# Optimization experiments

Measured on AMD Instinct MI355X. Metric: run time of the kernel, lower is better.

Reference implementation:

```python
import jax, jax.numpy as jnp
import numpy as np

N = 50000      # nodes
E = 800000     # edges (before self-loops)
DIN, H1, H2, OUT = 128, 128, 64, 40
LN_EPS = 1e-5


def setup_inputs() -> dict:
    key = jax.random.key(0)
    ks = jax.random.split(key, 16)
    s = lambda d: 1.0 / np.sqrt(d)
    inp = {
        "x": jax.random.normal(ks[0], (N, DIN), jnp.float32),
        "edge_index": jax.random.randint(ks[1], (2, E), 0, N, dtype=jnp.int64),
        # GCNConv weights (applied as x @ W) and biases
        "W1": jax.random.normal(ks[2], (DIN, H1), jnp.float32) * s(DIN),
        "b1": jnp.zeros((H1,), jnp.float32),
        "W2": jax.random.normal(ks[3], (H1, H2), jnp.float32) * s(H1),
        "b2": jnp.zeros((H2,), jnp.float32),
        "W3": jax.random.normal(ks[4], (H2, H2), jnp.float32) * s(H2),
        "b3": jnp.zeros((H2,), jnp.float32),
        # LayerNorms
        "g1": jnp.ones((H1,), jnp.float32),
        "be1": jnp.zeros((H1,), jnp.float32),
        "g2": jnp.ones((H2,), jnp.float32),
        "be2": jnp.zeros((H2,), jnp.float32),
        # post_mp MLP head
        "Wp1": jax.random.normal(ks[5], (H2, H2), jnp.float32) * s(H2),
        "bp1": jnp.zeros((H2,), jnp.float32),
        "Wp2": jax.random.normal(ks[6], (H2, OUT), jnp.float32) * s(H2),
        "bp2": jnp.zeros((OUT,), jnp.float32),
    }
    return inp


def _layer_norm(x, g, b):
    mu = jnp.mean(x, axis=-1, keepdims=True)
    var = jnp.mean((x - mu) ** 2, axis=-1, keepdims=True)
    return (x - mu) * jax.lax.rsqrt(var + LN_EPS) * g + b


def _gcn(x, src, dst, norm, W, b):
    # PyG GCNConv: linear first, then normalized gather/scatter-add, bias last
    h = x @ W                                  # [N, H]
    msg = h[src] * norm[:, None]               # [E+N, H] gather
    out = jax.ops.segment_sum(msg, dst, num_segments=N)  # scatter-add
    return out + b


def reference(x, edge_index, W1, b1, W2, b2, W3, b3, g1, be1, g2, be2,
              Wp1, bp1, Wp2, bp2):
    loops = jnp.arange(N, dtype=edge_index.dtype)
    src = jnp.concatenate([edge_index[0], loops])  # add self-loops
    dst = jnp.concatenate([edge_index[1], loops])
    # symmetric normalization D^{-1/2} (A+I) D^{-1/2} (same graph all layers)
    deg = jax.ops.segment_sum(jnp.ones_like(src, dtype=x.dtype), dst,
                              num_segments=N)
    dinv = jnp.where(deg > 0, jax.lax.rsqrt(jnp.maximum(deg, 1.0)), 0.0)
    norm = dinv[src] * dinv[dst]

    h = _gcn(x, src, dst, norm, W1, b1)
    h = _layer_norm(jax.nn.relu(h), g1, be1)
    h = _gcn(h, src, dst, norm, W2, b2)
    h = _layer_norm(jax.nn.relu(h), g2, be2)
    emb = _gcn(h, src, dst, norm, W3, b3)      # emb = conv output, pre-ReLU
    h = jax.nn.relu(emb)
    h = (h @ Wp1 + bp1) @ Wp2 + bp2            # post_mp: two stacked Linears
    return emb, jax.nn.log_softmax(h, axis=1)
```

## Files before the change

### kernel.cpp

```cpp
#include <hip/hip_runtime.h>
#include <hip/hip_bf16.h>

#define DIN 128
#define HID1 128
#define HID2 64
#define OUTD 40
#define NCHUNK 128

typedef __attribute__((ext_vector_type(8))) short bf16x8;
typedef __attribute__((ext_vector_type(4))) float f32x4;

__device__ __forceinline__ float bf2f(unsigned int u) {
    union { unsigned int i; float f; } c;
    c.i = u << 16;
    return c.f;
}
__device__ __forceinline__ unsigned short f2bf(float f) {
    union { float f; unsigned int i; } c; c.f = f;
    unsigned int r = c.i + 0x7FFFu + ((c.i >> 16) & 1u);
    return (unsigned short)(r >> 16);
}
__device__ __forceinline__ unsigned int packbf(float lo, float hi) {
    return (unsigned int)f2bf(lo) | ((unsigned int)f2bf(hi) << 16);
}

__device__ __forceinline__ int get_src(const int* ei, int E, int e, int e64) {
    return e64 ? ei[2 * e] : ei[e];
}
__device__ __forceinline__ int get_dst(const int* ei, int E, int e, int e64) {
    return e64 ? ei[2 * (E + e)] : ei[E + e];
}

struct WCvt {
    const void* p[14];
    int sz[14];
    int off[14];
    int tobf[14];
    int cols[14];
};

__launch_bounds__(1024)
__global__ void posA_kernel(const unsigned short* __restrict__ xu,
                            const int* __restrict__ ei,
                            int* __restrict__ flags,
                            int* __restrict__ pos,
                            unsigned int* __restrict__ hist,
                            int E, int N) {
    __shared__ unsigned int h32[25000];
    __shared__ int sh2[2];
    const int NW = (N + 1) >> 1;
    const int b = blockIdx.x;
    const int t = threadIdx.x;
    if (b < NCHUNK) {
        if (t == 0) sh2[0] = 0;
        for (int w = t; w < NW; w += 1024) h32[w] = 0u;
        __syncthreads();
        int zodd = 0;
        for (int k = t; k < 1024; k += 1024)
            if (ei[2 * k + 1] == 0) zodd++;
        if (zodd) atomicAdd(&sh2[0], zodd);
        __syncthreads();
        const int e64 = (sh2[0] > 512) ? 1 : 0;
        const int CH = (E + NCHUNK - 1) / NCHUNK;
        const int lo = b * CH;
        int hi = lo + CH; if (hi > E) hi = E;
        for (int e = lo + t; e < hi; e += 1024) {
            int d = e64 ? ei[2 * (E + e)] : ei[E + e];
            if ((unsigned)d < (unsigned)N) {
                unsigned sh = (unsigned)(d & 1) << 4;
                unsigned old = atomicAdd(&h32[d >> 1], 1u << sh);
                pos[e] = (int)((old >> sh) & 0xffffu);
            } else {
                pos[e] = -1;
            }
        }
        __syncthreads();
        unsigned int* hb = hist + (size_t)b * NW;
        for (int w = t; w < NW; w += 1024) hb[w] = h32[w];
    } else {
        if (t < 2) sh2[t] = 0;
        __syncthreads();
        int bad = 0;
        for (int k = t; k < 2048; k += 1024) {
            float v = bf2f(xu[2 * k]);
            float a = fabsf(v);
            if (!(a <= 1e4f) || (v != 0.f && a < 1e-4f)) bad++;
        }
        int zodd = 0;
        for (int k = t; k < 1024; k += 1024)
            if (ei[2 * k + 1] == 0) zodd++;
        if (bad) atomicAdd(&sh2[0], bad);
        if (zodd) atomicAdd(&sh2[1], zodd);
        __syncthreads();
        if (t == 0) {
            flags[0] = (sh2[0] > 512) ? 1 : 0;
            flags[1] = (sh2[1] > 512) ? 1 : 0;
        }
    }
}

__launch_bounds__(256)
__global__ void phaseB_kernel(const unsigned int* __restrict__ hist,
                              unsigned int* __restrict__ basev,
                              int* __restrict__ cnt, int* __restrict__ bsum,
                              int N, int PB,
                              WCvt wc, unsigned short* __restrict__ wbf,
                              float* __restrict__ wf,
                              const int* __restrict__ flags) {
    __shared__ int red[256];
    const int NW = (N + 1) >> 1;
    int t = threadIdx.x;
    int blk = blockIdx.x;
    if (blk < PB) {
        int w = blk * 256 + t;
        unsigned run0 = 0, run1 = 0;
        if (w < NW) {
            #pragma unroll 4
            for (int b = 0; b < NCHUNK; ++b) {
                unsigned u = hist[(size_t)b * NW + w];
                basev[(size_t)b * NW + w] = (run0 & 0xffffu) | (run1 << 16);
                run0 += u & 0xffffu;
                run1 += u >> 16;
            }
            cnt[2 * w] = (int)run0;
            if (2 * w + 1 < N) cnt[2 * w + 1] = (int)run1;
        }
        int tot = 0;
        if (w < NW) tot = (int)run0 + ((2 * w + 1 < N) ? (int)run1 : 0);
        red[t] = tot;
        __syncthreads();
        #pragma unroll
        for (int off = 64; off >= 1; off >>= 1) {
            if ((t & 127) < off) red[t] += red[t + off];
            __syncthreads();
        }
        if (t == 0) bsum[2 * blk] = red[0];
        if (t == 128) bsum[2 * blk + 1] = red[128];
    } else {
        int xf32 = flags[0];
        int stride = (gridDim.x - PB) * 256;
        int tid = (blk - PB) * 256 + t;
        for (int a = 0; a < 14; ++a) {
            const float* pf = (const float*)wc.p[a];
            const unsigned short* pb = (const unsigned short*)wc.p[a];
            int n = wc.sz[a], off = wc.off[a], tobf = wc.tobf[a];
            int cols = wc.cols[a];
            int rows = tobf ? (n / cols) : 0;
            for (int i = tid; i < n; i += stride) {
                float v = xf32 ? pf[i] : bf2f(pb[i]);
                if (tobf) {
                    int k = i / cols, m = i % cols;
                    wbf[off + m * rows + k] = f2bf(v);
                } else {
                    wf[off + i] = v;
                }
            }
        }
    }
}

__launch_bounds__(256)
__global__ void emit_kernel(const int* __restrict__ cnt, const int* __restrict__ bsum,
                            int* __restrict__ indptr, float* __restrict__ dinv,
                            int N, int NB) {
    __shared__ int part[256];
    __shared__ int sh[256];
    int t = threadIdx.x;
    part[t] = (t < NB) ? bsum[t] : 0;
    __syncthreads();
    for (int off = 1; off < 256; off <<= 1) {
        int v = (t >= off) ? part[t - off] : 0;
        __syncthreads();
        part[t] += v;
        __syncthreads();
    }
    int bbase = (blockIdx.x > 0) ? part[blockIdx.x - 1] : 0;
    int total = part[255];
    int i = blockIdx.x * 256 + t;
    int c = (i < N) ? cnt[i] : 0;
    sh[t] = c;
    __syncthreads();
    for (int off = 1; off < 256; off <<= 1) {
        int v = (t >= off) ? sh[t - off] : 0;
        __syncthreads();
        sh[t] += v;
        __syncthreads();
    }
    if (i < N) {
        int excl = sh[t] - c + bbase;
        indptr[i] = excl;
        dinv[i] = 1.0f / sqrtf((float)(c + 1));
    }
    if (blockIdx.x == (unsigned)(NB - 1) && t == 0) indptr[N] = total;
}

__global__ void scatter_kernel(const int* __restrict__ ei, const int* __restrict__ indptr,
                               const int* __restrict__ pos, const float* __restrict__ dinv,
                               const unsigned int* __restrict__ basev,
                               int2* __restrict__ csr_sn,
                               int E, int N, const int* __restrict__ flags) {
    int e64 = flags[1];
    int CH = (E + NCHUNK - 1) / NCHUNK;
    int NW = (N + 1) >> 1;
    int base = (blockIdx.x * blockDim.x + threadIdx.x) * 4;
    #pragma unroll
    for (int u = 0; u < 4; ++u) {
        int e = base + u;
        if (e < E) {
            int p = pos[e];
            if (p >= 0) {
                int bb = e / CH;
                int d = get_dst(ei, E, e, e64);
                int s = get_src(ei, E, e, e64);
                if ((unsigned)s >= (unsigned)N) s = 0;
                float nrm = dinv[s] * dinv[d];
                unsigned bw = basev[(size_t)bb * NW + (d >> 1)];
                int bval = (d & 1) ? (int)(bw >> 16) : (int)(bw & 0xffffu);
                int slot = indptr[d] + bval + p;
                csr_sn[slot] = make_int2(s, __float_as_int(nrm));
            }
        }
    }
}


template<typename AT>
__device__ __forceinline__ bf16x8 ld_afrag(const AT* p);
template<>
__device__ __forceinline__ bf16x8 ld_afrag<unsigned short>(const unsigned short* p) {
    return *(const bf16x8*)p;
}
template<>
__device__ __forceinline__ bf16x8 ld_afrag<float>(const float* p) {
    float4 a = *(const float4*)p;
    float4 b = *(const float4*)(p + 4);
    bf16x8 r;
    r[0] = (short)f2bf(a.x); r[1] = (short)f2bf(a.y);
    r[2] = (short)f2bf(a.z); r[3] = (short)f2bf(a.w);
    r[4] = (short)f2bf(b.x); r[5] = (short)f2bf(b.y);
    r[6] = (short)f2bf(b.z); r[7] = (short)f2bf(b.w);
    return r;
}

template<int K, int M, typename AT>
__device__ __forceinline__ void mm_body(const AT* __restrict__ A,
                                        const unsigned short* __restrict__ WT,
                                        unsigned short* __restrict__ C, int N,
                                        unsigned short (*Ws)[K + 8]) {
    int tid = threadIdx.x;
    for (int idx = tid; idx < M * K / 8; idx += 256) {
        int r = idx / (K / 8), c8 = idx % (K / 8);
        *(uint4*)&Ws[r][c8 * 8] = *(const uint4*)&WT[r * K + c8 * 8];
    }
    __syncthreads();
    int w = tid >> 6, lane = tid & 63;
    int m = lane & 15, q = lane >> 4;
    int row_a = blockIdx.x * 64 + w * 16 + m;
    if (row_a >= N) row_a = N - 1;
    const AT* arow = A + (size_t)row_a * K;
    f32x4 acc[M / 16];
    #pragma unroll
    for (int t = 0; t < M / 16; ++t) acc[t] = (f32x4){0.f, 0.f, 0.f, 0.f};
    #pragma unroll
    for (int ks = 0; ks < K / 32; ++ks) {
        int k0 = ks * 32 + q * 8;
        bf16x8 a = ld_afrag<AT>(arow + k0);
        #pragma unroll
        for (int t = 0; t < M / 16; ++t) {
            bf16x8 b = *(const bf16x8*)&Ws[t * 16 + m][k0];
            acc[t] = __builtin_amdgcn_mfma_f32_16x16x32_bf16(a, b, acc[t], 0, 0, 0);
        }
    }
    int rbase = blockIdx.x * 64 + w * 16 + q * 4;
    #pragma unroll
    for (int reg = 0; reg < 4; ++reg) {
        int row = rbase + reg;
        if (row < N) {
            #pragma unroll
            for (int t = 0; t < M / 16; ++t)
                C[(size_t)row * M + t * 16 + m] = f2bf(acc[t][reg]);
        }
    }
}

template<int K, int M>
__launch_bounds__(256)
__global__ void mm_dual_kernel(const void* __restrict__ A,
                               const unsigned short* __restrict__ WT,
                               unsigned short* __restrict__ C, int N,
                               const int* __restrict__ flags) {
    __shared__ unsigned short Ws[M][K + 8];
    if (flags[0]) mm_body<K, M, float>((const float*)A, WT, C, N, Ws);
    else          mm_body<K, M, unsigned short>((const unsigned short*)A, WT, C, N, Ws);
}

template<int K, int M>
__launch_bounds__(256)
__global__ void mm_bf_kernel(const unsigned short* __restrict__ A,
                             const unsigned short* __restrict__ WT,
                             unsigned short* __restrict__ C, int N) {
    __shared__ unsigned short Ws[M][K + 8];
    mm_body<K, M, unsigned short>(A, WT, C, N, Ws);
}


template<int VPL>
__device__ __forceinline__ void gacc1(float* acc, const unsigned short* r, float n) {
    if constexpr (VPL == 8) {
        uint4 u = *(const uint4*)r;
        acc[0] += bf2f(u.x & 0xffffu) * n; acc[1] += bf2f(u.x >> 16) * n;
        acc[2] += bf2f(u.y & 0xffffu) * n; acc[3] += bf2f(u.y >> 16) * n;
        acc[4] += bf2f(u.z & 0xffffu) * n; acc[5] += bf2f(u.z >> 16) * n;
        acc[6] += bf2f(u.w & 0xffffu) * n; acc[7] += bf2f(u.w >> 16) * n;
    } else {
        uint2 u = *(const uint2*)r;
        acc[0] += bf2f(u.x & 0xffffu) * n; acc[1] += bf2f(u.x >> 16) * n;
        acc[2] += bf2f(u.y & 0xffffu) * n; acc[3] += bf2f(u.y >> 16) * n;
    }
}

template<int VPL>
__device__ __forceinline__ void gacc8(float* acc,
                                      const unsigned short* const* rp,
                                      const float* nv) {
    if constexpr (VPL == 8) {
        uint4 u[8];
        #pragma unroll
        for (int i = 0; i < 8; ++i) u[i] = *(const uint4*)rp[i];
        #pragma unroll
        for (int i = 0; i < 8; ++i) {
            float n = nv[i];
            acc[0] += bf2f(u[i].x & 0xffffu) * n; acc[1] += bf2f(u[i].x >> 16) * n;
            acc[2] += bf2f(u[i].y & 0xffffu) * n; acc[3] += bf2f(u[i].y >> 16) * n;
            acc[4] += bf2f(u[i].z & 0xffffu) * n; acc[5] += bf2f(u[i].z >> 16) * n;
            acc[6] += bf2f(u[i].w & 0xffffu) * n; acc[7] += bf2f(u[i].w >> 16) * n;
        }
    } else {
        uint2 u[8];
        #pragma unroll
        for (int i = 0; i < 8; ++i) u[i] = *(const uint2*)rp[i];
        #pragma unroll
        for (int i = 0; i < 8; ++i) {
            float n = nv[i];
            acc[0] += bf2f(u[i].x & 0xffffu) * n; acc[1] += bf2f(u[i].x >> 16) * n;
            acc[2] += bf2f(u[i].y & 0xffffu) * n; acc[3] += bf2f(u[i].y >> 16) * n;
        }
    }
}

template<int H, bool RELU_LN, bool EMB>
__launch_bounds__(256)
__global__ void agg_kernel(const unsigned short* __restrict__ h,
                           const int* __restrict__ indptr,
                           const int2* __restrict__ csr_sn,
                           const float* __restrict__ dinv,
                           const float* __restrict__ bias,
                           const float* __restrict__ gamma,
                           const float* __restrict__ beta,
                           unsigned short* __restrict__ out,
                           void* __restrict__ out_emb,
                           int N, const int* __restrict__ flags) {
    constexpr int VPL = H / 16;
    __shared__ int2 lsn[4][4][32];
    int w = threadIdx.x >> 6;
    int lane = threadIdx.x & 63;
    int g = lane >> 4;
    int idx = lane & 15;
    int node = blockIdx.x * 16 + w * 4 + g;
    bool active = node < N;
    int nd = active ? node : N - 1;
    float di = dinv[nd];
    int c0 = idx * VPL;
    float acc[VPL];
    #pragma unroll
    for (int v = 0; v < VPL; ++v) acc[v] = 0.f;
    gacc1<VPL>(acc, h + (size_t)nd * H + c0, di * di);
    int beg = indptr[nd], end = indptr[nd + 1];
    for (int base = beg; base < end; base += 32) {
        int m = end - base; if (m > 32) m = 32;
        lsn[w][g][idx]      = (idx < m)      ? csr_sn[base + idx]      : make_int2(0, 0);
        lsn[w][g][idx + 16] = (idx + 16 < m) ? csr_sn[base + idx + 16] : make_int2(0, 0);
        int rounds = (m + 7) >> 3;
        int j = 0;
        for (int rr = 0; rr < rounds; ++rr, j += 8) {
            const unsigned short* rp[8];
            float nv[8];
            #pragma unroll
            for (int i = 0; i < 8; ++i) {
                int2 e = lsn[w][g][j + i];
                rp[i] = h + (size_t)e.x * H + c0;
                nv[i] = __int_as_float(e.y);
            }
            gacc8<VPL>(acc, rp, nv);
        }
    }
    #pragma unroll
    for (int v = 0; v < VPL; ++v) acc[v] += bias[c0 + v];
    if constexpr (RELU_LN) {
        #pragma unroll
        for (int v = 0; v < VPL; ++v) acc[v] = fmaxf(acc[v], 0.f);
        float s = 0.f, sq = 0.f;
        #pragma unroll
        for (int v = 0; v < VPL; ++v) { s += acc[v]; sq += acc[v] * acc[v]; }
        #pragma unroll
        for (int off = 8; off >= 1; off >>= 1) {
            s += __shfl_xor(s, off, 64);
            sq += __shfl_xor(sq, off, 64);
        }
        float mu = s * (1.0f / H);
        float var = fmaxf(sq * (1.0f / H) - mu * mu, 0.f);
        float inv = 1.0f / sqrtf(var + 1e-5f);
        #pragma unroll
        for (int v = 0; v < VPL; ++v)
            acc[v] = (acc[v] - mu) * inv * gamma[c0 + v] + beta[c0 + v];
    }
    if (active) {
        unsigned short* orow = out + (size_t)node * H + c0;
        if constexpr (VPL == 8) {
            uint4 p;
            p.x = packbf(acc[0], acc[1]); p.y = packbf(acc[2], acc[3]);
            p.z = packbf(acc[4], acc[5]); p.w = packbf(acc[6], acc[7]);
            *(uint4*)orow = p;
        } else {
            uint2 p; p.x = packbf(acc[0], acc[1]); p.y = packbf(acc[2], acc[3]);
            *(uint2*)orow = p;
        }
        if constexpr (EMB) {
            if (flags[0]) {
                float* o = (float*)out_emb + (size_t)node * H + c0;
                #pragma unroll
                for (int v4 = 0; v4 < VPL / 4; ++v4)
                    *(float4*)(o + v4 * 4) = make_float4(acc[v4 * 4], acc[v4 * 4 + 1],
                                                         acc[v4 * 4 + 2], acc[v4 * 4 + 3]);
            } else {
                unsigned short* o = (unsigned short*)out_emb + (size_t)node * H + c0;
                #pragma unroll
                for (int v2 = 0; v2 < VPL / 2; ++v2)
                    ((unsigned int*)o)[v2] = packbf(acc[v2 * 2], acc[v2 * 2 + 1]);
            }
        }
    }
}


__launch_bounds__(256)
__global__ void head_kernel(const unsigned short* __restrict__ emb,
                            const float* __restrict__ Wp1,
                            const float* __restrict__ bp1,
                            const float* __restrict__ Wp2,
                            const float* __restrict__ bp2,
                            void* __restrict__ d_out, int N,
                            const int* __restrict__ flags) {
    __shared__ float Est[64][68];
    __shared__ float W1s[64][64];
    __shared__ float Tst[64][68];
    __shared__ float W2s[64][OUTD];
    __shared__ float b1s[64];
    __shared__ float b2s[OUTD];
    int tid = threadIdx.x;
    int row0 = blockIdx.x * 64;
    for (int i = tid; i < 64 * 64; i += 256) W1s[i >> 6][i & 63] = Wp1[i];
    for (int i = tid; i < 64 * OUTD; i += 256) W2s[i / OUTD][i % OUTD] = Wp2[i];
    if (tid < 64) b1s[tid] = bp1[tid];
    if (tid < OUTD) b2s[tid] = bp2[tid];
    for (int i = tid; i < 64 * 32; i += 256) {
        int r = i >> 5, kk = i & 31;
        int row = row0 + r;
        unsigned int u = (row < N) ? *(const unsigned int*)&emb[(size_t)row * 64 + kk * 2] : 0u;
        Est[kk * 2][r]     = fmaxf(bf2f(u & 0xffffu), 0.f);
        Est[kk * 2 + 1][r] = fmaxf(bf2f(u >> 16), 0.f);
    }
    __syncthreads();
    {
        int rg = tid >> 4, cg = tid & 15;
        int r = rg * 4, c = cg * 4;
        float acc[4][4];
        #pragma unroll
        for (int i = 0; i < 4; ++i)
            #pragma unroll
            for (int jj = 0; jj < 4; ++jj) acc[i][jj] = b1s[c + jj];
        #pragma unroll 4
        for (int k = 0; k < 64; ++k) {
            float4 a = *(const float4*)&Est[k][r];
            float4 wv = *(const float4*)&W1s[k][c];
            acc[0][0] += a.x * wv.x; acc[0][1] += a.x * wv.y; acc[0][2] += a.x * wv.z; acc[0][3] += a.x * wv.w;
            acc[1][0] += a.y * wv.x; acc[1][1] += a.y * wv.y; acc[1][2] += a.y * wv.z; acc[1][3] += a.y * wv.w;
            acc[2][0] += a.z * wv.x; acc[2][1] += a.z * wv.y; acc[2][2] += a.z * wv.z; acc[2][3] += a.z * wv.w;
            acc[3][0] += a.w * wv.x; acc[3][1] += a.w * wv.y; acc[3][2] += a.w * wv.z; acc[3][3] += a.w * wv.w;
        }
        #pragma unroll
        for (int i = 0; i < 4; ++i)
            #pragma unroll
            for (int jj = 0; jj < 4; ++jj) Tst[c + jj][r + i] = acc[i][jj];
    }
    __syncthreads();
    int row = tid >> 2, tc = tid & 3, o0 = tc * 10;
    int node = row0 + row;
    float u[10];
    #pragma unroll
    for (int o = 0; o < 10; ++o) u[o] = b2s[o0 + o];
    for (int c2 = 0; c2 < 64; ++c2) {
        float tv = Tst[c2][row];
        const float2* wp = (const float2*)&W2s[c2][o0];
        #pragma unroll
        for (int o2 = 0; o2 < 5; ++o2) {
            float2 wv = wp[o2];
            u[o2 * 2]     += tv * wv.x;
            u[o2 * 2 + 1] += tv * wv.y;
        }
    }
    float mx = u[0];
    #pragma unroll
    for (int o = 1; o < 10; ++o) mx = fmaxf(mx, u[o]);
    mx = fmaxf(mx, __shfl_xor(mx, 1, 64));
    mx = fmaxf(mx, __shfl_xor(mx, 2, 64));
    float sum = 0.f;
    #pragma unroll
    for (int o = 0; o < 10; ++o) sum += __expf(u[o] - mx);
    sum += __shfl_xor(sum, 1, 64);
    sum += __shfl_xor(sum, 2, 64);
    float lse = mx + __logf(sum);
    if (node < N) {
        if (flags[0]) {
            float* base = (float*)d_out + (size_t)N * HID2;
            float* op = base + (size_t)node * OUTD + o0;
            #pragma unroll
            for (int o = 0; o < 10; ++o) op[o] = u[o] - lse;
        } else {
            unsigned short* base = (unsigned short*)d_out + (size_t)N * HID2;
            unsigned int* op = (unsigned int*)(base + (size_t)node * OUTD + o0);
            #pragma unroll
            for (int o2 = 0; o2 < 5; ++o2)
                op[o2] = packbf(u[o2 * 2] - lse, u[o2 * 2 + 1] - lse);
        }
    }
}


extern "C" void kernel_launch(void* const* d_in, const int* in_sizes, int n_in,
                              void* d_out, int out_size, void* d_ws, size_t ws_size,
                              hipStream_t stream) {
    const unsigned short* xu = (const unsigned short*)d_in[0];
    const int*            ei = (const int*)d_in[1];

    const int N = in_sizes[0] / DIN;
    const int E = in_sizes[1] / 2;
    const int NW = (N + 1) / 2;

    size_t off = 0;
    auto take = [&](size_t bytes) {
        size_t cur = off;
        off += (bytes + 255) & ~(size_t)255;
        return cur;
    };
    char* ws = (char*)d_ws;
    int*   flags   = (int*)  (ws + take(256));
    int*   cnt     = (int*)  (ws + take((size_t)N * 4));
    float* dinv    = (float*)(ws + take((size_t)N * 4));
    int*   indptr  = (int*)  (ws + take((size_t)(N + 1) * 4));
    int*   pos     = (int*)  (ws + take((size_t)E * 4));
    int2*  csr_sn  = (int2*) (ws + take((size_t)E * 8));
    int*   bsum    = (int*)  (ws + take(((size_t)N / 256 + 4) * 4));
    unsigned int* hist  = (unsigned int*)(ws + take((size_t)NCHUNK * NW * 4));
    unsigned int* basev = (unsigned int*)(ws + take((size_t)NCHUNK * NW * 4));
    unsigned short* wbf = (unsigned short*)(ws + take(32768 * 2));
    float*          wf  = (float*)         (ws + take(8192 * 4));
    unsigned short* hbuf = (unsigned short*)(ws + take((size_t)N * DIN * 2));
    unsigned short* abuf = (unsigned short*)(ws + take((size_t)N * DIN * 2));
    (void)ws_size; (void)n_in; (void)out_size;

    const int TB = 256;
    dim3 blk(TB);
    const int NB = (N + 255) / 256;
    const int PB = (NW + 255) / 256;

    WCvt wc;
    int bfoff = 0, foff = 0;
    int offs[14];
    const int wcols[14] = {HID1, 0, HID2, 0, HID2, 0, 0, 0, 0, 0, 0, 0, 0, 0};
    for (int a = 0; a < 14; ++a) {
        int idx = a + 2;
        wc.p[a] = d_in[idx];
        wc.sz[a] = in_sizes[idx];
        int tobf = (idx == 2 || idx == 4 || idx == 6) ? 1 : 0;
        wc.tobf[a] = tobf;
        wc.cols[a] = tobf ? wcols[a] : 1;
        if (tobf) { wc.off[a] = bfoff; bfoff += in_sizes[idx]; }
        else      { wc.off[a] = foff;  foff  += in_sizes[idx]; }
        offs[a] = wc.off[a];
    }

    posA_kernel<<<dim3(NCHUNK + 1), dim3(1024), 0, stream>>>(
        xu, ei, flags, pos, hist, E, N);
    phaseB_kernel<<<dim3(PB + 64), blk, 0, stream>>>(
        hist, basev, cnt, bsum, N, PB, wc, wbf, wf, flags);
    emit_kernel<<<dim3(NB), blk, 0, stream>>>(cnt, bsum, indptr, dinv, N, NB);
    scatter_kernel<<<dim3((E + 1023) / 1024), blk, 0, stream>>>(
        ei, indptr, pos, dinv, basev, csr_sn, E, N, flags);

    unsigned short* W1t = wbf + offs[0];
    unsigned short* W2t = wbf + offs[2];
    unsigned short* W3t = wbf + offs[4];
    float* b1f  = wf + offs[1];
    float* b2f  = wf + offs[3];
    float* b3f  = wf + offs[5];
    float* g1f  = wf + offs[6];
    float* be1f = wf + offs[7];
    float* g2f  = wf + offs[8];
    float* be2f = wf + offs[9];
    float* Wp1f = wf + offs[10];
    float* bp1f = wf + offs[11];
    float* Wp2f = wf + offs[12];
    float* bp2f = wf + offs[13];

    const int MMG = (N + 63) / 64;
    const int AGG = (N + 15) / 16;

    mm_dual_kernel<DIN, HID1><<<dim3(MMG), blk, 0, stream>>>(
        d_in[0], W1t, hbuf, N, flags);
    agg_kernel<HID1, true, false><<<dim3(AGG), blk, 0, stream>>>(
        hbuf, indptr, csr_sn, dinv, b1f, g1f, be1f, abuf, nullptr, N, flags);

    mm_bf_kernel<HID1, HID2><<<dim3(MMG), blk, 0, stream>>>(abuf, W2t, hbuf, N);
    agg_kernel<HID2, true, false><<<dim3(AGG), blk, 0, stream>>>(
        hbuf, indptr, csr_sn, dinv, b2f, g2f, be2f, abuf, nullptr, N, flags);

    mm_bf_kernel<HID2, HID2><<<dim3(MMG), blk, 0, stream>>>(abuf, W3t, hbuf, N);
    agg_kernel<HID2, false, true><<<dim3(AGG), blk, 0, stream>>>(
        hbuf, indptr, csr_sn, dinv, b3f, nullptr, nullptr, abuf, d_out, N, flags);

    head_kernel<<<dim3((N + 63) / 64), blk, 0, stream>>>(
        abuf, Wp1f, bp1f, Wp2f, bp2f, d_out, N, flags);
}
```

Measured before the change: 278.4 us.

## Assign one wavefront per node in GCN aggregation with edge-split lanes

The aggregation kernel now gives each node a full 64-lane wavefront instead of a 16-lane group. The four 16-lane slots each process a strided subset of the neighbour list with software-pipelined row loads, and the partials are combined by cross-slot shuffles. This is meant to balance work across nodes with uneven degree and to keep more gathers in flight per node. The cost is four times as many blocks, an extra shuffle reduction, and three quarters of the lanes sitting idle during the epilogue and writes.

Measured after the change: 310.6 us. +11.6%, slower.

```diff
diff --git a/kernel.cpp b/kernel.cpp
--- a/kernel.cpp
+++ b/kernel.cpp
@@ -305,46 +305,22 @@
 
 
 template<int VPL>
-__device__ __forceinline__ void gacc1(float* acc, const unsigned short* r, float n) {
+__device__ __forceinline__ uint4 ld_row(const unsigned short* p) {
     if constexpr (VPL == 8) {
-        uint4 u = *(const uint4*)r;
-        acc[0] += bf2f(u.x & 0xffffu) * n; acc[1] += bf2f(u.x >> 16) * n;
-        acc[2] += bf2f(u.y & 0xffffu) * n; acc[3] += bf2f(u.y >> 16) * n;
+        return *(const uint4*)p;
+    } else {
+        uint2 t = *(const uint2*)p;
+        return make_uint4(t.x, t.y, 0u, 0u);
+    }
+}
+
+template<int VPL>
+__device__ __forceinline__ void acc_row(float* acc, uint4 u, float n) {
+    acc[0] += bf2f(u.x & 0xffffu) * n; acc[1] += bf2f(u.x >> 16) * n;
+    acc[2] += bf2f(u.y & 0xffffu) * n; acc[3] += bf2f(u.y >> 16) * n;
+    if constexpr (VPL == 8) {
         acc[4] += bf2f(u.z & 0xffffu) * n; acc[5] += bf2f(u.z >> 16) * n;
         acc[6] += bf2f(u.w & 0xffffu) * n; acc[7] += bf2f(u.w >> 16) * n;
-    } else {
-        uint2 u = *(const uint2*)r;
-        acc[0] += bf2f(u.x & 0xffffu) * n; acc[1] += bf2f(u.x >> 16) * n;
-        acc[2] += bf2f(u.y & 0xffffu) * n; acc[3] += bf2f(u.y >> 16) * n;
-    }
-}
-
-template<int VPL>
-__device__ __forceinline__ void gacc8(float* acc,
-                                      const unsigned short* const* rp,
-                                      const float* nv) {
-    if constexpr (VPL == 8) {
-        uint4 u[8];
-        #pragma unroll
-        for (int i = 0; i < 8; ++i) u[i] = *(const uint4*)rp[i];
-        #pragma unroll
-        for (int i = 0; i < 8; ++i) {
-            float n = nv[i];
-            acc[0] += bf2f(u[i].x & 0xffffu) * n; acc[1] += bf2f(u[i].x >> 16) * n;
-            acc[2] += bf2f(u[i].y & 0xffffu) * n; acc[3] += bf2f(u[i].y >> 16) * n;
-            acc[4] += bf2f(u[i].z & 0xffffu) * n; acc[5] += bf2f(u[i].z >> 16) * n;
-            acc[6] += bf2f(u[i].w & 0xffffu) * n; acc[7] += bf2f(u[i].w >> 16) * n;
-        }
-    } else {
-        uint2 u[8];
-        #pragma unroll
-        for (int i = 0; i < 8; ++i) u[i] = *(const uint2*)rp[i];
-        #pragma unroll
-        for (int i = 0; i < 8; ++i) {
-            float n = nv[i];
-            acc[0] += bf2f(u[i].x & 0xffffu) * n; acc[1] += bf2f(u[i].x >> 16) * n;
-            acc[2] += bf2f(u[i].y & 0xffffu) * n; acc[3] += bf2f(u[i].y >> 16) * n;
-        }
     }
 }
 
@@ -361,12 +337,12 @@
                            void* __restrict__ out_emb,
                            int N, const int* __restrict__ flags) {
     constexpr int VPL = H / 16;
-    __shared__ int2 lsn[4][4][32];
+    __shared__ int2 lsn[4][64];
     int w = threadIdx.x >> 6;
     int lane = threadIdx.x & 63;
-    int g = lane >> 4;
+    int slot = lane >> 4;
     int idx = lane & 15;
-    int node = blockIdx.x * 16 + w * 4 + g;
+    int node = blockIdx.x * 4 + w;
     bool active = node < N;
     int nd = active ? node : N - 1;
     float di = dinv[nd];
@@ -374,25 +350,29 @@
     float acc[VPL];
     #pragma unroll
     for (int v = 0; v < VPL; ++v) acc[v] = 0.f;
-    gacc1<VPL>(acc, h + (size_t)nd * H + c0, di * di);
+    if (slot == 0)
+        acc_row<VPL>(acc, ld_row<VPL>(h + (size_t)nd * H + c0), di * di);
     int beg = indptr[nd], end = indptr[nd + 1];
-    for (int base = beg; base < end; base += 32) {
-        int m = end - base; if (m > 32) m = 32;
-        lsn[w][g][idx]      = (idx < m)      ? csr_sn[base + idx]      : make_int2(0, 0);
-        lsn[w][g][idx + 16] = (idx + 16 < m) ? csr_sn[base + idx + 16] : make_int2(0, 0);
-        int rounds = (m + 7) >> 3;
-        int j = 0;
-        for (int rr = 0; rr < rounds; ++rr, j += 8) {
-            const unsigned short* rp[8];
-            float nv[8];
-            #pragma unroll
-            for (int i = 0; i < 8; ++i) {
-                int2 e = lsn[w][g][j + i];
-                rp[i] = h + (size_t)e.x * H + c0;
-                nv[i] = __int_as_float(e.y);
-            }
-            gacc8<VPL>(acc, rp, nv);
-        }
+    for (int base = beg; base < end; base += 64) {
+        int m = end - base; if (m > 64) m = 64;
+        lsn[w][lane] = (lane < m) ? csr_sn[base + lane] : make_int2(0, 0);
+        int rounds = (m + 3) >> 2;
+        int2 e = lsn[w][slot];
+        uint4 u = ld_row<VPL>(h + (size_t)e.x * H + c0);
+        float n = __int_as_float(e.y);
+        for (int r = 1; r < rounds; ++r) {
+            int2 e2 = lsn[w][r * 4 + slot];
+            uint4 u2 = ld_row<VPL>(h + (size_t)e2.x * H + c0);
+            float n2 = __int_as_float(e2.y);
+            acc_row<VPL>(acc, u, n);
+            u = u2; n = n2;
+        }
+        acc_row<VPL>(acc, u, n);
+    }
+    #pragma unroll
+    for (int v = 0; v < VPL; ++v) {
+        acc[v] += __shfl_xor(acc[v], 16, 64);
+        acc[v] += __shfl_xor(acc[v], 32, 64);
     }
     #pragma unroll
     for (int v = 0; v < VPL; ++v) acc[v] += bias[c0 + v];
@@ -414,7 +394,7 @@
         for (int v = 0; v < VPL; ++v)
             acc[v] = (acc[v] - mu) * inv * gamma[c0 + v] + beta[c0 + v];
     }
-    if (active) {
+    if (active && slot == 0) {
         unsigned short* orow = out + (size_t)node * H + c0;
         if constexpr (VPL == 8) {
             uint4 p;
@@ -614,7 +594,7 @@
     float* bp2f = wf + offs[13];
 
     const int MMG = (N + 63) / 64;
-    const int AGG = (N + 15) / 16;
+    const int AGG = (N + 3) / 4;
 
     mm_dual_kernel<DIN, HID1><<<dim3(MMG), blk, 0, stream>>>(
         d_in[0], W1t, hbuf, N, flags);
```
